# Kernel optimization log

Hardware: AMD Instinct MI355X
Metric: run time of the kernel (lower is better)

Reference implementation:

```python
import jax, jax.numpy as jnp
import numpy as np

MAX_FREQ = 4
OMEGA = 0.5 * np.pi
PATCH = 64


def _unnorm(c, size):
    # align_corners=False convention of torch.grid_sample
    return ((c + 1.0) * size - 1.0) / 2.0


def _gather(im, yy, xx):
    # im [C,H,W], yy/xx [Ho,Wo] -> [C,Ho,Wo]
    return im[:, yy, xx]


def _gs_nearest(inp, grid):
    # inp [B,C,H,W], grid [B,Ho,Wo,2] (x,y); padding_mode='border'
    B, C, H, W = inp.shape
    x = jnp.clip(jnp.round(_unnorm(grid[..., 0], W)), 0, W - 1).astype(jnp.int32)
    y = jnp.clip(jnp.round(_unnorm(grid[..., 1], H)), 0, H - 1).astype(jnp.int32)
    return jax.vmap(_gather)(inp, y, x)  # [B,C,Ho,Wo]


def _gs_bilinear(inp, grid):
    B, C, H, W = inp.shape
    x = jnp.clip(_unnorm(grid[..., 0], W), 0.0, W - 1.0)
    y = jnp.clip(_unnorm(grid[..., 1], H), 0.0, H - 1.0)
    x0 = jnp.floor(x); y0 = jnp.floor(y)
    wx = (x - x0)[:, None]; wy = (y - y0)[:, None]  # [B,1,Ho,Wo]
    x0i = x0.astype(jnp.int32); y0i = y0.astype(jnp.int32)
    x1i = jnp.minimum(x0i + 1, W - 1); y1i = jnp.minimum(y0i + 1, H - 1)
    g = jax.vmap(_gather)
    v00 = g(inp, y0i, x0i); v01 = g(inp, y0i, x1i)
    v10 = g(inp, y1i, x0i); v11 = g(inp, y1i, x1i)
    return (v00 * (1 - wx) * (1 - wy) + v01 * wx * (1 - wy)
            + v10 * (1 - wx) * wy + v11 * wx * wy)


def _conv2d(x, w, b):
    y = jax.lax.conv_general_dilated(x, w, (1, 1), ((1, 1), (1, 1)),
                                     dimension_numbers=("NCHW", "OIHW", "NCHW"))
    return y + b[None, :, None, None]


def _lc_decoder(q, rel):
    # q [B,Ho,Wo,2F+1], rel [B,Ho,Wo,1]; Fourier basis [1, cos(k*w*rel), sin(k*w*rel)]
    k = jnp.arange(1, MAX_FREQ + 1, dtype=q.dtype)
    ang = rel * k * OMEGA  # [B,Ho,Wo,F]
    basis = jnp.concatenate([jnp.ones_like(rel), jnp.cos(ang), jnp.sin(ang)], axis=-1)
    return jnp.sum(q * basis, axis=-1, keepdims=True)  # [B,Ho,Wo,1]


def _forward(sinogram, feat, grid, square_inv, adapt_w, adapt_b):
    B = feat.shape[0]
    sino = _conv2d(feat, adapt_w, adapt_b)          # [B,2F+1,V,D]
    V, D = sino.shape[-2], sino.shape[-1]
    # make_coord along detector axis (dim=1 coord channel), padding=0
    coord_d = ((jnp.arange(D, dtype=sino.dtype) + 0.5) / D) * 2.0 - 1.0
    sino_coord = jnp.broadcast_to(coord_d[None, None, None, :], (B, 1, V, D))
    shift_interval = 1.0 / D
    eps = 1e-4
    q_recons, lengths = [], []
    for sx in (-shift_interval, shift_interval):  # ensembling shifts
        g = grid + jnp.array([sx, 0.0], dtype=grid.dtype) + 1e-6
        q_recon = jnp.transpose(_gs_nearest(sino, g), (0, 2, 3, 1))       # [B,V,P2,2F+1]
        q_coord = jnp.transpose(_gs_nearest(sino_coord, g), (0, 2, 3, 1))  # [B,V,P2,1]
        rel = (grid[..., 0:1] - q_coord) * D
        q_recons.append(_lc_decoder(q_recon, rel))
        lengths.append(jnp.abs(rel) + eps)
    tot = lengths[0] + lengths[1]
    # lengths are swapped before weighting (cross weighting)
    recon = q_recons[0] * lengths[1] / tot + q_recons[1] * lengths[0] / tot
    out = jnp.sum(jnp.transpose(recon, (0, 3, 1, 2)) * square_inv * 10000.0, axis=-2)
    # back projection of center channel of raw sinogram
    ch = sinogram.shape[1]
    bp = _gs_bilinear(sinogram[:, ch // 2:ch // 2 + 1], grid)
    out = out + jnp.sum(bp * square_inv * 10000.0, axis=-2)  # [B,1,P2]
    return out.reshape(B, 1, PATCH, PATCH)


def setup_inputs() -> dict:
    key = jax.random.key(0)
    ks = jax.random.split(key, 6)
    B, V, D, ENC = 4, 360, 512, 64
    P2 = PATCH * PATCH
    CH = 2 * MAX_FREQ + 1
    return {
        "sinogram": jax.random.normal(ks[0], (B, 1, V, D), jnp.float32),
        "feat": jax.random.normal(ks[1], (B, ENC, V, D), jnp.float32),
        "grid": jax.random.uniform(ks[2], (B, V, P2, 2), jnp.float32, -1.0, 1.0),
        "square_inv": jax.random.uniform(ks[3], (B, 1, V, P2), jnp.float32, 1e-5, 1e-4),
        "adapt_w": jax.random.normal(ks[4], (CH, ENC, 3, 3), jnp.float32) * 0.05,
        "adapt_b": jax.random.normal(ks[5], (CH,), jnp.float32) * 0.05,
    }


def reference(sinogram, feat, grid, square_inv, adapt_w, adapt_b):
    return _forward(sinogram, feat, grid, square_inv, adapt_w, adapt_b)
```

## Files before the change

kernel.cpp:

```cpp
#include <hip/hip_runtime.h>
#include <hip/hip_fp16.h>
#include <math.h>

#define B   4
#define V   360
#define D   512
#define ENC 64
#define CH  9
#define P2  4096
#define NCHUNK 90
#define VCHUNK 4
#define RECH 16
#define PENT 513
#define PENTB 64

template <int PAIR>
__global__ __launch_bounds__(256) void conv_kernel(
    const float* __restrict__ feat,
    const float* __restrict__ w,
    const float* __restrict__ bias,
    char* __restrict__ outp)
{
    const int bid = blockIdx.x;
    const int sw  = (bid & 7) * 180 + (bid >> 3);
    const int b   = sw / V;
    const int v   = sw % V;
    const int d0  = threadIdx.x * 2;

    float acc[CH][2];
    #pragma unroll
    for (int oc = 0; oc < CH; ++oc) {
        const float bv = bias[oc];
        acc[oc][0] = bv; acc[oc][1] = bv;
    }

    const float* fb = feat + ((size_t)b * ENC * V + v) * D + d0;
    const bool vm = v > 0, vp = v < V - 1;
    const bool dm = d0 > 0, dp = d0 + 2 < D;

    float r0[3][4], r1[3][4];

    auto ld = [&](float r[3][4], int ic) {
        const float* f = fb + (size_t)ic * (V * D);
        #pragma unroll
        for (int rr = 0; rr < 3; ++rr) {
            const float* fr = f + (rr - 1) * D;
            const bool ok = (rr == 0) ? vm : ((rr == 2) ? vp : true);
            float2 c = ok ? *(const float2*)fr : float2{0.f, 0.f};
            r[rr][1] = c.x; r[rr][2] = c.y;
            r[rr][0] = (ok && dm) ? fr[-1] : 0.f;
            r[rr][3] = (ok && dp) ? fr[2]  : 0.f;
        }
    };
    auto fmab = [&](const float r[3][4], int ic) {
        #pragma unroll
        for (int oc = 0; oc < CH; ++oc) {
            const float* ww = w + ((size_t)oc * ENC + ic) * 9;
            #pragma unroll
            for (int kr = 0; kr < 3; ++kr) {
                #pragma unroll
                for (int kc = 0; kc < 3; ++kc) {
                    const float wv = ww[kr * 3 + kc];
                    acc[oc][0] = fmaf(r[kr][kc],     wv, acc[oc][0]);
                    acc[oc][1] = fmaf(r[kr][kc + 1], wv, acc[oc][1]);
                }
            }
        }
    };

    ld(r0, 0);
    #pragma unroll 1
    for (int ic = 0; ic < ENC; ic += 2) {
        ld(r1, ic + 1);
        fmab(r0, ic);
        if (ic + 2 < ENC) ld(r0, ic + 2);
        fmab(r1, ic + 1);
    }

    #pragma unroll
    for (int p = 0; p < 2; ++p) {
        union { __half2 h; unsigned u; } cv;
        uint4 pk;
        cv.h = __floats2half2_rn(acc[0][p], acc[1][p]); pk.x = cv.u;
        cv.h = __floats2half2_rn(acc[2][p], acc[3][p]); pk.y = cv.u;
        cv.h = __floats2half2_rn(acc[4][p], acc[5][p]); pk.z = cv.u;
        cv.h = __floats2half2_rn(acc[6][p], acc[7][p]); pk.w = cv.u;
        cv.h = __floats2half2_rn(acc[8][p], 0.f);
        const unsigned short z = (unsigned short)(cv.u & 0xffffu);
        const int x = d0 + p;
        if (PAIR) {
            char* row = outp + (size_t)(b * V + v) * PENT * PENTB;
            char* eA = row + (size_t)(x + 1) * PENTB;
            *(uint4*)eA = pk;
            *(unsigned short*)(eA + 32) = z;
            char* eB = row + (size_t)x * PENTB + 16;
            *(uint4*)eB = pk;
            *(unsigned short*)(eB + 18) = z;
            if (x == 0) {
                *(uint4*)row = pk;
                *(unsigned short*)(row + 32) = z;
            }
            if (x == D - 1) {
                char* eC = row + (size_t)512 * PENTB + 16;
                *(uint4*)eC = pk;
                *(unsigned short*)(eC + 18) = z;
            }
        } else {
            __half* rec = (__half*)outp + (size_t)(((size_t)b * V + v) * D + x) * RECH;
            *(uint4*)rec = pk;
            *(unsigned*)(rec + 8) = (unsigned)z;
        }
    }
}

__global__ __launch_bounds__(256) void build_sg2(
    const float* __restrict__ sg, float2* __restrict__ sg2)
{
    const int i = blockIdx.x * 256 + threadIdx.x;
    const int x = i & (D - 1);
    const float a = sg[i];
    const float c = (x == D - 1) ? a : sg[i + 1];
    sg2[i] = float2{a, c};
}

__device__ __forceinline__ float decode_rec(uint4 a, unsigned short z, float rel)
{
    float q[9];
    union { unsigned uu; __half2 h; } c;
    float2 f;
    c.uu = a.x; f = __half22float2(c.h); q[0] = f.x; q[1] = f.y;
    c.uu = a.y; f = __half22float2(c.h); q[2] = f.x; q[3] = f.y;
    c.uu = a.z; f = __half22float2(c.h); q[4] = f.x; q[5] = f.y;
    c.uu = a.w; f = __half22float2(c.h); q[6] = f.x; q[7] = f.y;
    union { unsigned short us; __half hh; } c2;
    c2.us = z;
    q[8] = __half2float(c2.hh);

    const float ang = rel * 1.5707963267948966f;
    float s1, c1;
    __sincosf(ang, &s1, &c1);
    const float c2f = fmaf(2.f * c1, c1, -1.f);
    const float s2f = 2.f * c1 * s1;
    const float c3f = fmaf(2.f * c1, c2f, -c1);
    const float s3f = fmaf(2.f * c1, s2f, -s1);
    const float c4f = fmaf(2.f * c1, c3f, -c2f);
    const float s4f = fmaf(2.f * c1, s3f, -s2f);

    float vv = q[0];
    vv = fmaf(q[1], c1,  vv); vv = fmaf(q[2], c2f, vv);
    vv = fmaf(q[3], c3f, vv); vv = fmaf(q[4], c4f, vv);
    vv = fmaf(q[5], s1,  vv); vv = fmaf(q[6], s2f, vv);
    vv = fmaf(q[7], s3f, vv); vv = fmaf(q[8], s4f, vv);
    return vv;
}

__global__ __launch_bounds__(256) void sample_pair(
    const char* __restrict__ pair,
    const float2* __restrict__ sg2,
    const float* __restrict__ grid,
    const float* __restrict__ sq,
    float* __restrict__ partial)
{
    const int bid = blockIdx.x;
    const int xcd = bid & 7;
    const int b   = xcd >> 1;
    const int idx = ((bid >> 3) << 1) | (xcd & 1);
    const int chunk = idx >> 4;
    const int p  = (idx & 15) * 256 + threadIdx.x;
    const int v0 = chunk * VCHUNK;

    const char*   pb  = pair + (size_t)b * V * PENT * PENTB;
    const float2* s2b = sg2 + (size_t)b * V * D;

    float gx[4], gy[4], sv[4];
    #pragma unroll
    for (int u = 0; u < 4; ++u) {
        const size_t gi = (size_t)(b * V + v0 + u) * P2 + p;
        const double gd = __builtin_nontemporal_load((const double*)grid + gi);
        const unsigned long long gu = __double_as_longlong(gd);
        gx[u] = __uint_as_float((unsigned)gu);
        gy[u] = __uint_as_float((unsigned)(gu >> 32));
        sv[u] = __builtin_nontemporal_load(sq + gi);
    }

    uint4 qa[4], qb[4];
    unsigned short zA[4], zB[4];
    float relm[4], relp[4];
    #pragma unroll
    for (int u = 0; u < 4; ++u) {
        const float fy = ((gy[u] + 1e-6f + 1.f) * (float)V - 1.f) * 0.5f;
        const int   yi = (int)fminf(fmaxf(rintf(fy), 0.f), (float)(V - 1));
        const float fx0 = ((gx[u] + 1e-6f + 1.f) * (float)D - 1.f) * 0.5f;
        const int xm = (int)fminf(fmaxf(rintf(fx0 - 0.5f), 0.f), (float)(D - 1));
        const int xp = (int)fminf(fmaxf(rintf(fx0 + 0.5f), 0.f), (float)(D - 1));
        const float qcm = ((float)xm + 0.5f) * (2.f / (float)D) - 1.f;
        const float qcp = ((float)xp + 0.5f) * (2.f / (float)D) - 1.f;
        relm[u] = (gx[u] - qcm) * (float)D;
        relp[u] = (gx[u] - qcp) * (float)D;
        const char* rowp = pb + (size_t)yi * (PENT * PENTB);
        const char* e1 = rowp + (size_t)(xm + 1) * PENTB;
        const char* e2 = rowp + (size_t)xp * PENTB;
        qa[u] = *(const uint4*)e1;
        zA[u] = *(const unsigned short*)(e1 + 32);
        qb[u] = *(const uint4*)(e2 + 16);
        zB[u] = *(const unsigned short*)(e2 + 34);
    }

    float bl00[4], bl01[4], bl10[4], bl11[4], wxv[4], wyv[4];
    #pragma unroll
    for (int u = 0; u < 4; ++u) {
        float fxb = fminf(fmaxf(((gx[u] + 1.f) * (float)D - 1.f) * 0.5f, 0.f), (float)(D - 1));
        float fyb = fminf(fmaxf(((gy[u] + 1.f) * (float)V - 1.f) * 0.5f, 0.f), (float)(V - 1));
        const float x0 = floorf(fxb), y0 = floorf(fyb);
        wxv[u] = fxb - x0; wyv[u] = fyb - y0;
        const int x0i = (int)x0, y0i = (int)y0;
        const int y1i = min(y0i + 1, V - 1);
        const float2 t  = s2b[y0i * D + x0i];
        const float2 u2 = s2b[y1i * D + x0i];
        bl00[u] = t.x;  bl01[u] = t.y;
        bl10[u] = u2.x; bl11[u] = u2.y;
    }

    float acc = 0.f;
    #pragma unroll
    for (int u = 0; u < 4; ++u) {
        const float vmv = decode_rec(qa[u], zA[u], relm[u]);
        const float vpv = decode_rec(qb[u], zB[u], relp[u]);
        const float lm = fabsf(relm[u]) + 1e-4f;
        const float lp = fabsf(relp[u]) + 1e-4f;
        const float recon = (vmv * lp + vpv * lm) / (lm + lp);

        const float wx = wxv[u], wy = wyv[u];
        const float bp = bl00[u] * (1.f - wx) * (1.f - wy) + bl01[u] * wx * (1.f - wy)
                       + bl10[u] * (1.f - wx) * wy         + bl11[u] * wx * wy;

        acc += (recon + bp) * sv[u] * 1e4f;
    }
    __builtin_nontemporal_store(acc, partial + ((size_t)chunk * B + b) * P2 + p);
}

template <int PAIRED>
__global__ __launch_bounds__(256) void sample_basic(
    const __half* __restrict__ sino,
    const float* __restrict__ sinogram,
    const float2* __restrict__ sg2,
    const float* __restrict__ grid,
    const float* __restrict__ sq,
    float* __restrict__ partial)
{
    const int bid = blockIdx.x;
    const int xcd = bid & 7;
    const int b   = xcd >> 1;
    const int idx = ((bid >> 3) << 1) | (xcd & 1);
    const int chunk = idx >> 4;
    const int p  = (idx & 15) * 256 + threadIdx.x;
    const int v0 = chunk * VCHUNK;

    const float*  sg   = sinogram + (size_t)b * V * D;
    const float2* s2b  = sg2 + (size_t)b * V * D;
    const __half* sb   = sino + (size_t)b * V * D * RECH;

    float gx[4], gy[4], sv[4];
    #pragma unroll
    for (int u = 0; u < 4; ++u) {
        const size_t gi = (size_t)(b * V + v0 + u) * P2 + p;
        const double gd = __builtin_nontemporal_load((const double*)grid + gi);
        const unsigned long long gu = __double_as_longlong(gd);
        gx[u] = __uint_as_float((unsigned)gu);
        gy[u] = __uint_as_float((unsigned)(gu >> 32));
        sv[u] = __builtin_nontemporal_load(sq + gi);
    }

    uint4    ra[4][2];
    unsigned rz[4][2];
    float    rel[4][2];
    #pragma unroll
    for (int u = 0; u < 4; ++u) {
        const float fy = ((gy[u] + 1e-6f + 1.f) * (float)V - 1.f) * 0.5f;
        const int   yi = (int)fminf(fmaxf(rintf(fy), 0.f), (float)(V - 1));
        const float fx0 = ((gx[u] + 1e-6f + 1.f) * (float)D - 1.f) * 0.5f;
        #pragma unroll
        for (int sft = 0; sft < 2; ++sft) {
            const float fx = (sft == 0) ? (fx0 - 0.5f) : (fx0 + 0.5f);
            const int   xi = (int)fminf(fmaxf(rintf(fx), 0.f), (float)(D - 1));
            const float qc = ((float)xi + 0.5f) * (2.f / (float)D) - 1.f;
            rel[u][sft] = (gx[u] - qc) * (float)D;
            const __half* rec = sb + (size_t)(yi * D + xi) * RECH;
            ra[u][sft] = *(const uint4*)rec;
            rz[u][sft] = *(const unsigned*)(rec + 8);
        }
    }

    float bl00[4], bl01[4], bl10[4], bl11[4], wxv[4], wyv[4];
    #pragma unroll
    for (int u = 0; u < 4; ++u) {
        float fxb = fminf(fmaxf(((gx[u] + 1.f) * (float)D - 1.f) * 0.5f, 0.f), (float)(D - 1));
        float fyb = fminf(fmaxf(((gy[u] + 1.f) * (float)V - 1.f) * 0.5f, 0.f), (float)(V - 1));
        const float x0 = floorf(fxb), y0 = floorf(fyb);
        wxv[u] = fxb - x0; wyv[u] = fyb - y0;
        const int x0i = (int)x0, y0i = (int)y0;
        const int y1i = min(y0i + 1, V - 1);
        if (PAIRED) {
            const float2 t  = s2b[y0i * D + x0i];
            const float2 u2 = s2b[y1i * D + x0i];
            bl00[u] = t.x;  bl01[u] = t.y;
            bl10[u] = u2.x; bl11[u] = u2.y;
        } else {
            const int x1i = min(x0i + 1, D - 1);
            bl00[u] = sg[y0i * D + x0i]; bl01[u] = sg[y0i * D + x1i];
            bl10[u] = sg[y1i * D + x0i]; bl11[u] = sg[y1i * D + x1i];
        }
    }

    float acc = 0.f;
    #pragma unroll
    for (int u = 0; u < 4; ++u) {
        const float v0f = decode_rec(ra[u][0], (unsigned short)(rz[u][0] & 0xffffu), rel[u][0]);
        const float v1f = decode_rec(ra[u][1], (unsigned short)(rz[u][1] & 0xffffu), rel[u][1]);
        const float l0 = fabsf(rel[u][0]) + 1e-4f;
        const float l1 = fabsf(rel[u][1]) + 1e-4f;
        const float recon = (v0f * l1 + v1f * l0) / (l0 + l1);
        const float wx = wxv[u], wy = wyv[u];
        const float bp = bl00[u] * (1.f - wx) * (1.f - wy) + bl01[u] * wx * (1.f - wy)
                       + bl10[u] * (1.f - wx) * wy         + bl11[u] * wx * wy;
        acc += (recon + bp) * sv[u] * 1e4f;
    }
    __builtin_nontemporal_store(acc, partial + ((size_t)chunk * B + b) * P2 + p);
}

__global__ __launch_bounds__(256) void reduce_kernel(
    const float* __restrict__ partial, float* __restrict__ out)
{
    const int i = blockIdx.x * 256 + threadIdx.x;
    float a = 0.f;
    #pragma unroll 6
    for (int c = 0; c < NCHUNK; ++c)
        a += __builtin_nontemporal_load(partial + (size_t)c * B * P2 + i);
    out[i] = a;
}

extern "C" void kernel_launch(void* const* d_in, const int* in_sizes, int n_in,
                              void* d_out, int out_size, void* d_ws, size_t ws_size,
                              hipStream_t stream)
{
    const float* sinogram = (const float*)d_in[0];
    const float* feat     = (const float*)d_in[1];
    const float* grid     = (const float*)d_in[2];
    const float* sq       = (const float*)d_in[3];
    const float* w        = (const float*)d_in[4];
    const float* bias     = (const float*)d_in[5];
    float* out = (float*)d_out;

    const size_t pair_b = (size_t)B * V * PENT * PENTB;
    const size_t part_b = (size_t)NCHUNK * B * P2 * sizeof(float);
    const size_t sg2_b  = (size_t)B * V * D * sizeof(float2);
    const size_t rec_b  = (size_t)B * V * D * RECH * sizeof(__half);

    if (ws_size >= pair_b + part_b + sg2_b) {
        char*   pair    = (char*)d_ws;
        float*  partial = (float*)((char*)d_ws + pair_b);
        float2* sg2     = (float2*)((char*)d_ws + pair_b + part_b);
        conv_kernel<1><<<dim3(1440), 256, 0, stream>>>(feat, w, bias, pair);
        build_sg2<<<dim3(2880), 256, 0, stream>>>(sinogram, sg2);
        sample_pair<<<dim3(5760), 256, 0, stream>>>(pair, sg2, grid, sq, partial);
        reduce_kernel<<<dim3((B * P2) / 256), 256, 0, stream>>>(partial, out);
    } else if (ws_size >= rec_b + part_b + sg2_b) {
        char*   sino    = (char*)d_ws;
        float*  partial = (float*)((char*)d_ws + rec_b);
        float2* sg2     = (float2*)((char*)d_ws + rec_b + part_b);
        conv_kernel<0><<<dim3(1440), 256, 0, stream>>>(feat, w, bias, sino);
        build_sg2<<<dim3(2880), 256, 0, stream>>>(sinogram, sg2);
        sample_basic<1><<<dim3(5760), 256, 0, stream>>>((const __half*)sino, sinogram, sg2, grid, sq, partial);
        reduce_kernel<<<dim3((B * P2) / 256), 256, 0, stream>>>(partial, out);
    } else {
        char*   sino    = (char*)d_ws;
        float*  partial = (float*)((char*)d_ws + rec_b);
        conv_kernel<0><<<dim3(1440), 256, 0, stream>>>(feat, w, bias, sino);
        sample_basic<0><<<dim3(5760), 256, 0, stream>>>((const __half*)sino, sinogram, (const float2*)sino, grid, sq, partial);
        reduce_kernel<<<dim3((B * P2) / 256), 256, 0, stream>>>(partial, out);
    }
}
```

Baseline: 315.0 us.

## Widen conv per-thread tile, precompute 2x2 bilinear quads, merge z loads

The convolution kernel now computes 8 output columns per thread with 64-thread blocks instead of 2 columns with 256 threads. This reuses each loaded feature row and weight across more outputs and uses float4 loads, at the cost of many more registers and one wave per block. The sinogram prep now stores a float4 per pixel holding all four bilinear neighbours, so the sampler does one gather instead of two. The sampler also merges the two fp16 tail loads when both entries coincide and adds scheduling barriers to keep the loads grouped ahead of the math.

```diff
diff --git a/kernel.cpp b/kernel.cpp
--- a/kernel.cpp
+++ b/kernel.cpp
@@ -15,7 +15,7 @@
 #define PENTB 64
 
 template <int PAIR>
-__global__ __launch_bounds__(256) void conv_kernel(
+__global__ __launch_bounds__(64) void conv_kernel(
     const float* __restrict__ feat,
     const float* __restrict__ w,
     const float* __restrict__ bias,
@@ -25,34 +25,37 @@
     const int sw  = (bid & 7) * 180 + (bid >> 3);
     const int b   = sw / V;
     const int v   = sw % V;
-    const int d0  = threadIdx.x * 2;
-
-    float acc[CH][2];
+    const int d0  = threadIdx.x * 8;
+
+    float acc[CH][8];
     #pragma unroll
     for (int oc = 0; oc < CH; ++oc) {
         const float bv = bias[oc];
-        acc[oc][0] = bv; acc[oc][1] = bv;
+        #pragma unroll
+        for (int p = 0; p < 8; ++p) acc[oc][p] = bv;
     }
 
     const float* fb = feat + ((size_t)b * ENC * V + v) * D + d0;
     const bool vm = v > 0, vp = v < V - 1;
-    const bool dm = d0 > 0, dp = d0 + 2 < D;
-
-    float r0[3][4], r1[3][4];
-
-    auto ld = [&](float r[3][4], int ic) {
+    const bool dm = d0 > 0, dp = d0 + 8 < D;
+
+    float r0[3][10], r1[3][10];
+
+    auto ld = [&](float r[3][10], int ic) {
         const float* f = fb + (size_t)ic * (V * D);
         #pragma unroll
         for (int rr = 0; rr < 3; ++rr) {
             const float* fr = f + (rr - 1) * D;
             const bool ok = (rr == 0) ? vm : ((rr == 2) ? vp : true);
-            float2 c = ok ? *(const float2*)fr : float2{0.f, 0.f};
-            r[rr][1] = c.x; r[rr][2] = c.y;
+            float4 c0 = ok ? *(const float4*)fr       : float4{0.f, 0.f, 0.f, 0.f};
+            float4 c1 = ok ? *(const float4*)(fr + 4) : float4{0.f, 0.f, 0.f, 0.f};
+            r[rr][1] = c0.x; r[rr][2] = c0.y; r[rr][3] = c0.z; r[rr][4] = c0.w;
+            r[rr][5] = c1.x; r[rr][6] = c1.y; r[rr][7] = c1.z; r[rr][8] = c1.w;
             r[rr][0] = (ok && dm) ? fr[-1] : 0.f;
-            r[rr][3] = (ok && dp) ? fr[2]  : 0.f;
+            r[rr][9] = (ok && dp) ? fr[8]  : 0.f;
         }
     };
-    auto fmab = [&](const float r[3][4], int ic) {
+    auto fmab = [&](const float r[3][10], int ic) {
         #pragma unroll
         for (int oc = 0; oc < CH; ++oc) {
             const float* ww = w + ((size_t)oc * ENC + ic) * 9;
@@ -61,8 +64,9 @@
                 #pragma unroll
                 for (int kc = 0; kc < 3; ++kc) {
                     const float wv = ww[kr * 3 + kc];
-                    acc[oc][0] = fmaf(r[kr][kc],     wv, acc[oc][0]);
-                    acc[oc][1] = fmaf(r[kr][kc + 1], wv, acc[oc][1]);
+                    #pragma unroll
+                    for (int p = 0; p < 8; ++p)
+                        acc[oc][p] = fmaf(r[kr][p + kc], wv, acc[oc][p]);
                 }
             }
         }
@@ -78,7 +82,7 @@
     }
 
     #pragma unroll
-    for (int p = 0; p < 2; ++p) {
+    for (int p = 0; p < 8; ++p) {
         union { __half2 h; unsigned u; } cv;
         uint4 pk;
         cv.h = __floats2half2_rn(acc[0][p], acc[1][p]); pk.x = cv.u;
@@ -113,6 +117,21 @@
     }
 }
 
+__global__ __launch_bounds__(256) void build_sg4(
+    const float* __restrict__ sg, float4* __restrict__ sg4)
+{
+    const int i  = blockIdx.x * 256 + threadIdx.x;
+    const int x  = i & (D - 1);
+    const int bv = i >> 9;
+    const int v  = bv % V;
+    const float a = sg[i];
+    const float c = (x < D - 1) ? sg[i + 1] : a;
+    const int i2 = (v < V - 1) ? i + D : i;
+    const float d2 = sg[i2];
+    const float e2 = (x < D - 1) ? sg[i2 + 1] : d2;
+    sg4[i] = float4{a, c, d2, e2};
+}
+
 __global__ __launch_bounds__(256) void build_sg2(
     const float* __restrict__ sg, float2* __restrict__ sg2)
 {
@@ -154,8 +173,10 @@
     return vv;
 }
 
+template <int SG4>
 __global__ __launch_bounds__(256) void sample_pair(
     const char* __restrict__ pair,
+    const float4* __restrict__ sg4,
     const float2* __restrict__ sg2,
     const float* __restrict__ grid,
     const float* __restrict__ sq,
@@ -170,6 +191,7 @@
     const int v0 = chunk * VCHUNK;
 
     const char*   pb  = pair + (size_t)b * V * PENT * PENTB;
+    const float4* s4b = sg4 + (size_t)b * V * D;
     const float2* s2b = sg2 + (size_t)b * V * D;
 
     float gx[4], gy[4], sv[4];
@@ -201,9 +223,11 @@
         const char* e1 = rowp + (size_t)(xm + 1) * PENTB;
         const char* e2 = rowp + (size_t)xp * PENTB;
         qa[u] = *(const uint4*)e1;
-        zA[u] = *(const unsigned short*)(e1 + 32);
         qb[u] = *(const uint4*)(e2 + 16);
-        zB[u] = *(const unsigned short*)(e2 + 34);
+        const unsigned zab = *(const unsigned*)(e1 + 32);
+        zA[u] = (unsigned short)(zab & 0xffffu);
+        zB[u] = (e2 == e1) ? (unsigned short)(zab >> 16)
+                           : *(const unsigned short*)(e2 + 34);
     }
 
     float bl00[4], bl01[4], bl10[4], bl11[4], wxv[4], wyv[4];
@@ -214,12 +238,19 @@
         const float x0 = floorf(fxb), y0 = floorf(fyb);
         wxv[u] = fxb - x0; wyv[u] = fyb - y0;
         const int x0i = (int)x0, y0i = (int)y0;
-        const int y1i = min(y0i + 1, V - 1);
-        const float2 t  = s2b[y0i * D + x0i];
-        const float2 u2 = s2b[y1i * D + x0i];
-        bl00[u] = t.x;  bl01[u] = t.y;
-        bl10[u] = u2.x; bl11[u] = u2.y;
-    }
+        if (SG4) {
+            const float4 t = s4b[y0i * D + x0i];
+            bl00[u] = t.x; bl01[u] = t.y; bl10[u] = t.z; bl11[u] = t.w;
+        } else {
+            const int y1i = min(y0i + 1, V - 1);
+            const float2 t  = s2b[y0i * D + x0i];
+            const float2 u2 = s2b[y1i * D + x0i];
+            bl00[u] = t.x;  bl01[u] = t.y;
+            bl10[u] = u2.x; bl11[u] = u2.y;
+        }
+    }
+
+    __builtin_amdgcn_sched_barrier(0);
 
     float acc = 0.f;
     #pragma unroll
@@ -312,6 +343,8 @@
         }
     }
 
+    __builtin_amdgcn_sched_barrier(0);
+
     float acc = 0.f;
     #pragma unroll
     for (int u = 0; u < 4; ++u) {
@@ -353,29 +386,38 @@
 
     const size_t pair_b = (size_t)B * V * PENT * PENTB;
     const size_t part_b = (size_t)NCHUNK * B * P2 * sizeof(float);
+    const size_t sg4_b  = (size_t)B * V * D * sizeof(float4);
     const size_t sg2_b  = (size_t)B * V * D * sizeof(float2);
     const size_t rec_b  = (size_t)B * V * D * RECH * sizeof(__half);
 
-    if (ws_size >= pair_b + part_b + sg2_b) {
+    if (ws_size >= pair_b + part_b + sg4_b) {
+        char*   pair    = (char*)d_ws;
+        float*  partial = (float*)((char*)d_ws + pair_b);
+        float4* sg4     = (float4*)((char*)d_ws + pair_b + part_b);
+        conv_kernel<1><<<dim3(1440), 64, 0, stream>>>(feat, w, bias, pair);
+        build_sg4<<<dim3(2880), 256, 0, stream>>>(sinogram, sg4);
+        sample_pair<1><<<dim3(5760), 256, 0, stream>>>(pair, sg4, (const float2*)sg4, grid, sq, partial);
+        reduce_kernel<<<dim3((B * P2) / 256), 256, 0, stream>>>(partial, out);
+    } else if (ws_size >= pair_b + part_b + sg2_b) {
         char*   pair    = (char*)d_ws;
         float*  partial = (float*)((char*)d_ws + pair_b);
         float2* sg2     = (float2*)((char*)d_ws + pair_b + part_b);
-        conv_kernel<1><<<dim3(1440), 256, 0, stream>>>(feat, w, bias, pair);
+        conv_kernel<1><<<dim3(1440), 64, 0, stream>>>(feat, w, bias, pair);
         build_sg2<<<dim3(2880), 256, 0, stream>>>(sinogram, sg2);
-        sample_pair<<<dim3(5760), 256, 0, stream>>>(pair, sg2, grid, sq, partial);
+        sample_pair<0><<<dim3(5760), 256, 0, stream>>>(pair, (const float4*)sg2, sg2, grid, sq, partial);
         reduce_kernel<<<dim3((B * P2) / 256), 256, 0, stream>>>(partial, out);
     } else if (ws_size >= rec_b + part_b + sg2_b) {
         char*   sino    = (char*)d_ws;
         float*  partial = (float*)((char*)d_ws + rec_b);
         float2* sg2     = (float2*)((char*)d_ws + rec_b + part_b);
-        conv_kernel<0><<<dim3(1440), 256, 0, stream>>>(feat, w, bias, sino);
+        conv_kernel<0><<<dim3(1440), 64, 0, stream>>>(feat, w, bias, sino);
         build_sg2<<<dim3(2880), 256, 0, stream>>>(sinogram, sg2);
         sample_basic<1><<<dim3(5760), 256, 0, stream>>>((const __half*)sino, sinogram, sg2, grid, sq, partial);
         reduce_kernel<<<dim3((B * P2) / 256), 256, 0, stream>>>(partial, out);
     } else {
         char*   sino    = (char*)d_ws;
         float*  partial = (float*)((char*)d_ws + rec_b);
-        conv_kernel<0><<<dim3(1440), 256, 0, stream>>>(feat, w, bias, sino);
+        conv_kernel<0><<<dim3(1440), 64, 0, stream>>>(feat, w, bias, sino);
         sample_basic<0><<<dim3(5760), 256, 0, stream>>>((const __half*)sino, sinogram, (const float2*)sino, grid, sq, partial);
         reduce_kernel<<<dim3((B * P2) / 256), 256, 0, stream>>>(partial, out);
     }
```

After: 330.1 us. 4.8% more time.
